# Kernel optimization log

Measured on AMD Instinct MI355X. Metric: run time of the kernel, lower is better.

The kernel has to match this reference:

```python
import jax, jax.numpy as jnp
import numpy as np

B, L, IN = 4, 2048, 64
D, N, K, NL, NC = 256, 16, 32, 2, 2


def _ln(x, g, b):
    m = x.mean(-1, keepdims=True)
    v = ((x - m) ** 2).mean(-1, keepdims=True)
    return (x - m) * jax.lax.rsqrt(v + 1e-5) * g + b


def _dwconv(x, w, b):
    # depthwise conv1d, kernel 3, padding 1; x: [B,L,D], w: [D,3]
    xp = jnp.pad(x, ((0, 0), (1, 1), (0, 0)))
    return xp[:, :-2] * w[:, 0] + xp[:, 1:-1] * w[:, 1] + xp[:, 2:] * w[:, 2] + b


def _ssm(x, loglam, wd, bd, wb, wc, wo, bo):
    # x: [B,L,D]
    lam = jax.nn.softplus(loglam)                      # [D,N]
    delta = jax.nn.softplus(x @ wd + bd)[..., None]    # [B,L,D,1]
    Bt = (x @ wb)[:, :, None, :]                       # [B,L,1,N]
    Ct = (x @ wc)[:, :, None, :]                       # [B,L,1,N]
    A_d = jnp.exp(-delta * lam)                        # [B,L,D,N]
    B_d = delta * Bt                                   # [B,L,D,N]
    A_l = jnp.moveaxis(A_d, 1, 0)                      # [L,B,D,N]
    B_l = jnp.moveaxis(B_d, 1, 0)

    def step(h, ab):
        a, b = ab
        h = a * h + b
        return h, h

    h0 = jnp.zeros((x.shape[0], D, N), x.dtype)
    _, hs = jax.lax.scan(step, h0, (A_l, B_l))         # [L,B,D,N]
    ys = hs * jnp.moveaxis(Ct, 1, 0)                   # [L,B,D,N]
    out = jnp.moveaxis(ys, 0, 1).reshape(x.shape[0], x.shape[1], D * N)
    return out @ wo + bo


def _temporal_block(x, lg, lb, cw, cb, loglam, wd, bd, wb, wc, wo, bo, gw, gb, pw, pb):
    res = x
    xn = _ln(x, lg, lb)
    xc = _dwconv(xn, cw, cb)
    xs = _ssm(xc, loglam, wd, bd, wb, wc, wo, bo)
    g = jax.nn.sigmoid(xn @ gw + gb)
    return (xs * g) @ pw + pb + res


def _spectral(x, fr, fi):
    X = jnp.fft.rfft(x, axis=1)                        # [B,F,D] complex64
    mag = jnp.abs(X).mean(axis=(0, 2))                 # [F]
    k = min(K, X.shape[1])
    _, idx = jax.lax.top_k(mag, k)
    filt = (fr[:, :k] + 1j * fi[:, :k]).T              # [k,D]
    Xk = X[:, idx, :] * filt[None]
    Xo = jnp.zeros(X.shape, X.dtype).at[:, idx, :].set(Xk)
    return jnp.fft.irfft(Xo, n=x.shape[1], axis=1)


def setup_inputs() -> dict:
    key = jax.random.key(0)
    ks = jax.random.split(key, 32)
    rn = lambda i, shape, s=0.02: jax.random.normal(ks[i], shape, jnp.float32) * s
    inp = {
        "x": jax.random.normal(ks[0], (B, L, IN), jnp.float32),
        "w_in": rn(1, (IN, D), 0.1), "b_in": jnp.zeros((D,), jnp.float32),
        "ln_g": jnp.ones((NL, D), jnp.float32), "ln_b": jnp.zeros((NL, D), jnp.float32),
        "conv_w": rn(2, (NL, D, 3), 0.3), "conv_b": jnp.zeros((NL, D), jnp.float32),
        "loglam": jax.random.uniform(ks[3], (NL, D, N), jnp.float32),
        "wd": rn(4, (NL, D, D), 0.05), "bd": jnp.zeros((NL, D), jnp.float32),
        "wb": rn(5, (NL, D, N), 0.05), "wc": rn(6, (NL, D, N), 0.05),
        "wo": rn(7, (NL, D * N, D), 0.01), "bo": jnp.zeros((NL, D), jnp.float32),
        "gate_w": rn(8, (NL, D, D), 0.05), "gate_b": jnp.zeros((NL, D), jnp.float32),
        "proj_w": rn(9, (NL, D, D), 0.05), "proj_b": jnp.zeros((NL, D), jnp.float32),
        "fr": rn(10, (D, K)), "fi": rn(11, (D, K)),
        "alpha": jnp.full((D,), 0.5, jnp.float32), "beta": jnp.full((D,), 0.5, jnp.float32),
        "g_out": jnp.ones((D,), jnp.float32), "b_out": jnp.zeros((D,), jnp.float32),
        "hw1": rn(12, (D, D // 2), 0.05), "hb1": jnp.zeros((D // 2,), jnp.float32),
        "hw2": rn(13, (D // 2, NC), 0.05), "hb2": jnp.zeros((NC,), jnp.float32),
    }
    return inp


def reference(x, w_in, b_in, ln_g, ln_b, conv_w, conv_b, loglam, wd, bd, wb, wc, wo, bo,
              gate_w, gate_b, proj_w, proj_b, fr, fi, alpha, beta, g_out, b_out,
              hw1, hb1, hw2, hb2):
    h = x @ w_in + b_in                                # [B,L,D]
    xt = h
    for i in range(NL):
        xt = _temporal_block(xt, ln_g[i], ln_b[i], conv_w[i], conv_b[i], loglam[i],
                             wd[i], bd[i], wb[i], wc[i], wo[i], bo[i],
                             gate_w[i], gate_b[i], proj_w[i], proj_b[i])
    xs = _spectral(h, fr, fi)
    z = alpha * xt + beta * xs
    z = _ln(z, g_out, b_out)
    zl = z[:, -1, :]                                   # [B,D]
    hid = jax.nn.silu(zl @ hw1 + hb1)                  # dropout is identity in eval
    return hid @ hw2 + hb2                             # [B,NC]
```

## Files before the change

### kernel.cpp

```cpp
#include <hip/hip_runtime.h>
#include <hip/hip_bf16.h>
#include <math.h>

#define BB   4
#define LL   2048
#define INF_ 64
#define DD   256
#define NN   16
#define KK   32
#define BLn  (BB*LL)
#define FCNT 1025
#define FSTR 1056
#define SKM  8192
#define SKN  256
#define PSZ  ((size_t)SKM * SKN)
#define IX(x) ((x) + ((x) >> 6))

typedef short short4v __attribute__((ext_vector_type(4)));
typedef short short8 __attribute__((ext_vector_type(8)));
typedef float f32x4  __attribute__((ext_vector_type(4)));

__device__ __forceinline__ float softplusf(float x) {
    return x > 20.f ? x : log1pf(__expf(x));
}
__device__ __forceinline__ float sigmoidf_(float x) {
    return 1.f / (1.f + __expf(-x));
}
__device__ __forceinline__ short bfs(float v) {
    __hip_bfloat16 h = __float2bfloat16(v);
    return *reinterpret_cast<short*>(&h);
}

__global__ void prep_kernel(const float* __restrict__ wd, const float* __restrict__ gw,
                            const float* __restrict__ pw, const float* __restrict__ wo,
                            const float* __restrict__ wb, const float* __restrict__ wc,
                            const float* __restrict__ w_in, float* __restrict__ tab,
                            __hip_bfloat16* __restrict__ cat0, __hip_bfloat16* __restrict__ cat1,
                            __hip_bfloat16* __restrict__ gwt, __hip_bfloat16* __restrict__ pwt,
                            __hip_bfloat16* __restrict__ wot, __hip_bfloat16* __restrict__ wint) {
    __shared__ float t[32][33];
    const int tid = threadIdx.x;
    int blk = blockIdx.x;
    if (blk < 8) {
        int i = blk * 256 + tid;
        if (i < 2048) {
            double ang = 2.0 * 3.14159265358979323846 * (double)i / 2048.0;
            tab[i]        = (float)cos(ang);
            tab[2048 + i] = (float)sin(ang);
        }
        return;
    }
    blk -= 8;
    const float* W; __hip_bfloat16* Wt; int K, N, bx, by;
    if (blk < 64)        { W = wd;                     Wt = cat0; K = 256;  N = 256; bx = blk & 7; by = blk >> 3; }
    else if (blk < 128)  { int q = blk - 64;  W = wd + 65536; Wt = cat1; K = 256; N = 256; bx = q & 7; by = q >> 3; }
    else if (blk < 192)  { int q = blk - 128; W = gw;  Wt = gwt;  K = 256;  N = 256; bx = q & 7; by = q >> 3; }
    else if (blk < 256)  { int q = blk - 192; W = pw;  Wt = pwt;  K = 256;  N = 256; bx = q & 7; by = q >> 3; }
    else if (blk < 1280) { int q = blk - 256; W = wo;  Wt = wot;  K = 4096; N = 256; bx = q & 7; by = q >> 3; }
    else if (blk < 1344) {
        int j = (blk - 1280) & 31;
        const float* src0 = (blk < 1312) ? wb : wb + DD * NN;
        const float* src1 = (blk < 1312) ? wc : wc + DD * NN;
        __hip_bfloat16* cat = (blk < 1312) ? cat0 : cat1;
        const float* src = (j < 16) ? src0 : src1;
        cat[(size_t)(256 + j) * 256 + tid] = __float2bfloat16(src[tid * 16 + (j & 15)]);
        return;
    } else { int q = blk - 1344; W = w_in; Wt = wint; K = 64; N = 256; bx = q & 7; by = q >> 3; }
    const int k0 = by * 32, n0 = bx * 32;
    if (k0 >= K) return;
    const int tx = tid & 31, ty = tid >> 5;
    for (int r = ty; r < 32; r += 8) t[r][tx] = W[(size_t)(k0 + r) * N + n0 + tx];
    __syncthreads();
    for (int r = ty; r < 32; r += 8)
        Wt[(size_t)(n0 + r) * K + k0 + tx] = __float2bfloat16(t[tx][r]);
}

__global__ __launch_bounds__(256)
void gemm_in_kernel(const float* __restrict__ x, const __hip_bfloat16* __restrict__ wint,
                    const float* __restrict__ b_in, float* __restrict__ h,
                    float* __restrict__ ht) {
    __shared__ alignas(16) short As[64][72];
    __shared__ alignas(16) short Bs[64][72];
    __shared__ float ts[64][68];
    const int tid = threadIdx.x;
    const int w = tid >> 6, lane = tid & 63;
    const int hi = lane >> 4, lo = lane & 15;
    const int row0 = blockIdx.y * 64, col0 = blockIdx.x * 64;
    const short* B = (const short*)wint;
#pragma unroll
    for (int e = 0; e < 4; ++e) {
        int q = e * 256 + tid;
        int r = q >> 4, c4 = (q & 15) * 4;
        float4 v = *(const float4*)&x[(size_t)(row0 + r) * 64 + c4];
        short4v s = {bfs(v.x), bfs(v.y), bfs(v.z), bfs(v.w)};
        *(short4v*)&As[r][c4] = s;
    }
#pragma unroll
    for (int e = 0; e < 2; ++e) {
        int q = e * 256 + tid;
        int r = q >> 3, c8 = (q & 7) * 8;
        *(short8*)&Bs[r][c8] = *(const short8*)&B[(size_t)(col0 + r) * 64 + c8];
    }
    __syncthreads();
    f32x4 acc[4];
    f32x4 zz = {0.f, 0.f, 0.f, 0.f};
#pragma unroll
    for (int n = 0; n < 4; ++n) acc[n] = zz;
#pragma unroll
    for (int s = 0; s < 2; ++s) {
        short8 af = *(const short8*)&As[w * 16 + lo][s * 32 + hi * 8];
#pragma unroll
        for (int n = 0; n < 4; ++n) {
            short8 bf = *(const short8*)&Bs[n * 16 + lo][s * 32 + hi * 8];
            acc[n] = __builtin_amdgcn_mfma_f32_16x16x32_bf16(af, bf, acc[n], 0, 0, 0);
        }
    }
#pragma unroll
    for (int n = 0; n < 4; ++n)
#pragma unroll
        for (int r = 0; r < 4; ++r) {
            const int row = row0 + w * 16 + hi * 4 + r;
            const int col = col0 + n * 16 + lo;
            float v = acc[n][r] + b_in[col];
            h[(size_t)row * 256 + col] = v;
            ts[n * 16 + lo][w * 16 + hi * 4 + r] = v;
        }
    __syncthreads();
    const int b = row0 >> 11, l0 = row0 & 2047, d0 = col0;
    const int dr = tid >> 2, seg = tid & 3;
    float* dst = ht + ((size_t)(b * 256 + d0 + dr)) * LL + l0 + seg * 16;
#pragma unroll
    for (int j = 0; j < 4; ++j)
        *(f32x4*)&dst[j * 4] = *(const f32x4*)&ts[dr][seg * 16 + j * 4];
}

__global__ __launch_bounds__(256)
void lnconv_kernel(const float* __restrict__ X, const float* __restrict__ g,
                   const float* __restrict__ bln, const float* __restrict__ cw,
                   const float* __restrict__ cb, __hip_bfloat16* __restrict__ xn_bf,
                   __hip_bfloat16* __restrict__ xc_bf) {
    __shared__ float xs[34][260];
    const int tid = threadIdx.x;
    const int w = tid >> 6, lane = tid & 63;
    const int blk = blockIdx.x;
    const int b = (blk * 32) >> 11, L0 = (blk * 32) & 2047;
    const float4 g4 = *(const float4*)&g[lane * 4];
    const float4 b4 = *(const float4*)&bln[lane * 4];
    for (int slot = w; slot < 34; slot += 4) {
        const int l = L0 - 1 + slot;
        if (l < 0 || l >= LL) {
            f32x4 z = {0.f, 0.f, 0.f, 0.f};
            *(f32x4*)&xs[slot][lane * 4] = z;
            continue;
        }
        float4 v = *(const float4*)&X[((size_t)b * LL + l) * DD + lane * 4];
        float s = v.x + v.y + v.z + v.w;
#pragma unroll
        for (int off = 1; off < 64; off <<= 1) s += __shfl_xor(s, off);
        float m = s * (1.f / DD);
        float cx = v.x - m, cy = v.y - m, cz = v.z - m, cw_ = v.w - m;
        float q = cx * cx + cy * cy + cz * cz + cw_ * cw_;
#pragma unroll
        for (int off = 1; off < 64; off <<= 1) q += __shfl_xor(q, off);
        float inv = rsqrtf(q * (1.f / DD) + 1e-5f);
        f32x4 y;
        y[0] = cx * inv * g4.x + b4.x;
        y[1] = cy * inv * g4.y + b4.y;
        y[2] = cz * inv * g4.z + b4.z;
        y[3] = cw_ * inv * g4.w + b4.w;
        *(f32x4*)&xs[slot][lane * 4] = y;
        if (slot >= 1 && slot <= 32) {
            short4v s4 = {bfs(y[0]), bfs(y[1]), bfs(y[2]), bfs(y[3])};
            *(short4v*)&xn_bf[((size_t)b * LL + l) * DD + lane * 4] = s4;
        }
    }
    __syncthreads();
    const int d = tid;
    const float w0 = cw[d * 3 + 0], w1 = cw[d * 3 + 1], w2 = cw[d * 3 + 2], cbd = cb[d];
    float xm = xs[0][d], x0 = xs[1][d];
    for (int rw = 0; rw < 32; ++rw) {
        float xp = xs[rw + 2][d];
        xc_bf[((size_t)b * LL + L0 + rw) * DD + d] =
            __float2bfloat16(fmaf(w0, xm, fmaf(w1, x0, fmaf(w2, xp, cbd))));
        xm = x0; x0 = xp;
    }
}

template<int MODE>
__global__ __launch_bounds__(256)
void gemm_core(const short* __restrict__ A, const short* __restrict__ Bw,
               const float* __restrict__ bias, const float* __restrict__ x1,
               const float* __restrict__ x2, float* __restrict__ o0,
               float* __restrict__ o1, float* __restrict__ o2,
               __hip_bfloat16* __restrict__ ob) {
    __shared__ alignas(16) short As[2][64][40];
    __shared__ alignas(16) short Bs[2][64][40];
    const int tid = threadIdx.x;
    const int w = tid >> 6, lane = tid & 63;
    const int hi = lane >> 4, lo = lane & 15;
    const int row0 = blockIdx.y * 64, col0 = blockIdx.x * 64;
    f32x4 acc[4];
    f32x4 zz = {0.f, 0.f, 0.f, 0.f};
#pragma unroll
    for (int n = 0; n < 4; ++n) acc[n] = zz;
    const int sr = tid >> 2, sc = (tid & 3) * 8;
    short8 pa = *(const short8*)&A[(size_t)(row0 + sr) * 256 + sc];
    short8 pb = *(const short8*)&Bw[(size_t)(col0 + sr) * 256 + sc];
    *(short8*)&As[0][sr][sc] = pa;
    *(short8*)&Bs[0][sr][sc] = pb;
    pa = *(const short8*)&A[(size_t)(row0 + sr) * 256 + 32 + sc];
    pb = *(const short8*)&Bw[(size_t)(col0 + sr) * 256 + 32 + sc];
    __syncthreads();
    int cur = 0;
    for (int it = 0; it < 8; ++it) {
        if (it + 1 < 8) {
            *(short8*)&As[cur ^ 1][sr][sc] = pa;
            *(short8*)&Bs[cur ^ 1][sr][sc] = pb;
        }
        if (it + 2 < 8) {
            const int k0 = (it + 2) << 5;
            pa = *(const short8*)&A[(size_t)(row0 + sr) * 256 + k0 + sc];
            pb = *(const short8*)&Bw[(size_t)(col0 + sr) * 256 + k0 + sc];
        }
        short8 af = *(const short8*)&As[cur][w * 16 + lo][hi * 8];
        short8 bfr[4];
#pragma unroll
        for (int n = 0; n < 4; ++n)
            bfr[n] = *(const short8*)&Bs[cur][n * 16 + lo][hi * 8];
#pragma unroll
        for (int n = 0; n < 4; ++n)
            acc[n] = __builtin_amdgcn_mfma_f32_16x16x32_bf16(af, bfr[n], acc[n], 0, 0, 0);
        __syncthreads();
        cur ^= 1;
    }
#pragma unroll
    for (int n = 0; n < 4; ++n) {
#pragma unroll
        for (int r = 0; r < 4; ++r) {
            const int row = row0 + w * 16 + hi * 4 + r;
            const int col = col0 + n * 16 + lo;
            float v = acc[n][r];
            if constexpr (MODE == 0) {
                if (col < 256)      o0[(size_t)row * 256 + col] = softplusf(v + bias[col]);
                else if (col < 272) o1[(size_t)row * 16 + col - 256] = v;
                else if (col < 288) o2[(size_t)row * 16 + col - 272] = v;
            } else if constexpr (MODE == 1) {
                float gv = sigmoidf_(v + bias[col]);
                float s = x1[(size_t)row * 256 + col] + x1[PSZ + (size_t)row * 256 + col] + x2[col];
                ob[(size_t)row * 256 + col] = __float2bfloat16(gv * s);
            } else {
                o0[(size_t)row * 256 + col] = v + bias[col] + x1[(size_t)row * 256 + col];
            }
        }
    }
}

__global__ __launch_bounds__(256)
void gemm_sk_kernel(const __hip_bfloat16* __restrict__ Abf, const __hip_bfloat16* __restrict__ Wt,
                    float* __restrict__ P) {
    __shared__ alignas(16) short As[2][128][72];
    __shared__ alignas(16) short Bs[2][64][72];
    const int tid = threadIdx.x;
    const int f = blockIdx.x;
    const int xcd = f & 7, slot = f >> 3;
    const int col = slot & 3;
    const int rk = xcd + (slot >> 2) * 8;
    const int row = rk & 63, kb = rk >> 6;
    const int row0 = row * 128, col0 = col * 64;
    const size_t kbase = (size_t)kb * 2048;
    const int w = tid >> 6, lane = tid & 63;
    const int hi = lane >> 4, lo = lane & 15;
    const short* A = (const short*)Abf;
    const short* B = (const short*)Wt;
    f32x4 acc[2][4];
    f32x4 zz = {0.f, 0.f, 0.f, 0.f};
#pragma unroll
    for (int m = 0; m < 2; ++m)
#pragma unroll
        for (int n = 0; n < 4; ++n) acc[m][n] = zz;
    const int sr = tid >> 3, sc = (tid & 7) * 8;
    const int sr1 = (256 + tid) >> 3, sc1 = ((256 + tid) & 7) * 8;
    const int sr2 = (512 + tid) >> 3, sc2 = ((512 + tid) & 7) * 8;
    const int sr3 = (768 + tid) >> 3, sc3 = ((768 + tid) & 7) * 8;
    short8 pa0 = *(const short8*)&A[(size_t)(row0 + sr ) * 4096 + kbase + sc ];
    short8 pa1 = *(const short8*)&A[(size_t)(row0 + sr1) * 4096 + kbase + sc1];
    short8 pa2 = *(const short8*)&A[(size_t)(row0 + sr2) * 4096 + kbase + sc2];
    short8 pa3 = *(const short8*)&A[(size_t)(row0 + sr3) * 4096 + kbase + sc3];
    short8 pb0 = *(const short8*)&B[(size_t)(col0 + sr ) * 4096 + kbase + sc ];
    short8 pb1 = *(const short8*)&B[(size_t)(col0 + sr1) * 4096 + kbase + sc1];
    *(short8*)&As[0][sr ][sc ] = pa0;
    *(short8*)&As[0][sr1][sc1] = pa1;
    *(short8*)&As[0][sr2][sc2] = pa2;
    *(short8*)&As[0][sr3][sc3] = pa3;
    *(short8*)&Bs[0][sr ][sc ] = pb0;
    *(short8*)&Bs[0][sr1][sc1] = pb1;
    {
        const size_t k0 = kbase + 64;
        pa0 = *(const short8*)&A[(size_t)(row0 + sr ) * 4096 + k0 + sc ];
        pa1 = *(const short8*)&A[(size_t)(row0 + sr1) * 4096 + k0 + sc1];
        pa2 = *(const short8*)&A[(size_t)(row0 + sr2) * 4096 + k0 + sc2];
        pa3 = *(const short8*)&A[(size_t)(row0 + sr3) * 4096 + k0 + sc3];
        pb0 = *(const short8*)&B[(size_t)(col0 + sr ) * 4096 + k0 + sc ];
        pb1 = *(const short8*)&B[(size_t)(col0 + sr1) * 4096 + k0 + sc1];
    }
    __syncthreads();
    int cur = 0;
    for (int it = 0; it < 32; ++it) {
        if (it + 1 < 32) {
            *(short8*)&As[cur ^ 1][sr ][sc ] = pa0;
            *(short8*)&As[cur ^ 1][sr1][sc1] = pa1;
            *(short8*)&As[cur ^ 1][sr2][sc2] = pa2;
            *(short8*)&As[cur ^ 1][sr3][sc3] = pa3;
            *(short8*)&Bs[cur ^ 1][sr ][sc ] = pb0;
            *(short8*)&Bs[cur ^ 1][sr1][sc1] = pb1;
        }
        if (it + 2 < 32) {
            const size_t k0 = kbase + (size_t)(it + 2) * 64;
            pa0 = *(const short8*)&A[(size_t)(row0 + sr ) * 4096 + k0 + sc ];
            pa1 = *(const short8*)&A[(size_t)(row0 + sr1) * 4096 + k0 + sc1];
            pa2 = *(const short8*)&A[(size_t)(row0 + sr2) * 4096 + k0 + sc2];
            pa3 = *(const short8*)&A[(size_t)(row0 + sr3) * 4096 + k0 + sc3];
            pb0 = *(const short8*)&B[(size_t)(col0 + sr ) * 4096 + k0 + sc ];
            pb1 = *(const short8*)&B[(size_t)(col0 + sr1) * 4096 + k0 + sc1];
        }
#pragma unroll
        for (int kk = 0; kk < 2; ++kk) {
            short8 af[2], bfr[4];
#pragma unroll
            for (int m = 0; m < 2; ++m)
                af[m] = *(const short8*)&As[cur][w * 32 + m * 16 + lo][kk * 32 + hi * 8];
#pragma unroll
            for (int n = 0; n < 4; ++n)
                bfr[n] = *(const short8*)&Bs[cur][n * 16 + lo][kk * 32 + hi * 8];
#pragma unroll
            for (int m = 0; m < 2; ++m)
#pragma unroll
                for (int n = 0; n < 4; ++n)
                    acc[m][n] = __builtin_amdgcn_mfma_f32_16x16x32_bf16(af[m], bfr[n], acc[m][n], 0, 0, 0);
        }
        __syncthreads();
        cur ^= 1;
    }
    float* Pk = P + (size_t)kb * PSZ;
#pragma unroll
    for (int m = 0; m < 2; ++m)
#pragma unroll
        for (int n = 0; n < 4; ++n)
#pragma unroll
            for (int r = 0; r < 4; ++r) {
                int rr = row0 + w * 32 + m * 16 + hi * 4 + r;
                int cc = col0 + n * 16 + lo;
                Pk[(size_t)rr * SKN + cc] = acc[m][n][r];
            }
}

template<int PHASE>
__global__ void ssm_chunk_kernel(const float* __restrict__ delta, const float* __restrict__ Bt,
                                 const float* __restrict__ Ct, const float* __restrict__ loglam,
                                 const float* __restrict__ hstart,
                                 float* __restrict__ sA, float* __restrict__ sB,
                                 __hip_bfloat16* __restrict__ ys) {
    __shared__ float dl[128][16];
    __shared__ float btl[128][16];
    __shared__ float ctl[128][16];
    const int dblk = blockIdx.x, c = blockIdx.y, b = blockIdx.z;
    const int tid = threadIdx.x;
    const size_t lbase = (size_t)b * LL + c * 128;
    for (int i = tid; i < 2048; i += 256) {
        int l = i >> 4, q = i & 15;
        dl[l][q]  = delta[(lbase + l) * DD + dblk * 16 + q];
        btl[l][q] = Bt[(lbase + l) * NN + q];
        if (PHASE == 1) ctl[l][q] = Ct[(lbase + l) * NN + q];
    }
    __syncthreads();
    const int dloc = tid >> 4, n = tid & 15;
    const float lam = softplusf(loglam[(dblk * 16 + dloc) * NN + n]);
    float hv = 0.f, ap = 1.f;
    if (PHASE == 1) hv = hstart[((size_t)(b * 16 + c)) * 4096 + dblk * 256 + tid];
    for (int l = 0; l < 128; ++l) {
        float dv = dl[l][dloc];
        float a = __expf(-dv * lam);
        hv = fmaf(a, hv, dv * btl[l][n]);
        if (PHASE == 0) ap *= a;
        else ys[(lbase + l) * (DD * NN) + dblk * 256 + tid] = __float2bfloat16(hv * ctl[l][n]);
    }
    if (PHASE == 0) {
        size_t oi = ((size_t)(b * 16 + c)) * 4096 + dblk * 256 + tid;
        sA[oi] = ap; sB[oi] = hv;
    }
}

__global__ void ssm_comb_kernel(const float* __restrict__ sA, const float* __restrict__ sB,
                                float* __restrict__ hstart, float* __restrict__ hfin) {
    const int id = blockIdx.x * 256 + threadIdx.x;
    const int b = id >> 12, col = id & 4095;
    float h = 0.f;
#pragma unroll
    for (int c = 0; c < 16; ++c) {
        size_t oi = ((size_t)(b * 16 + c)) * 4096 + col;
        hstart[oi] = h;
        h = fmaf(sA[oi], h, sB[oi]);
    }
    if (hfin) hfin[(size_t)b * 4096 + col] = h;
}

__global__ void last_ssm_part_kernel(const float* __restrict__ hfin, const float* __restrict__ Ct,
                                     const float* __restrict__ wo, float* __restrict__ part) {
    __shared__ float hC[4][128];
    const int c = blockIdx.x, tid = threadIdx.x;
    const int p0 = c * 128;
#pragma unroll
    for (int e = 0; e < 2; ++e) {
        int i = e * 256 + tid;
        int b = i >> 7, p = i & 127;
        hC[b][p] = hfin[b * 4096 + p0 + p] *
                   Ct[((size_t)b * LL + (LL - 1)) * NN + (p & 15)];
    }
    __syncthreads();
    float a0 = 0.f, a1 = 0.f, a2 = 0.f, a3 = 0.f;
    for (int p = 0; p < 128; ++p) {
        float wv = wo[(size_t)(p0 + p) * DD + tid];
        a0 = fmaf(hC[0][p], wv, a0);
        a1 = fmaf(hC[1][p], wv, a1);
        a2 = fmaf(hC[2][p], wv, a2);
        a3 = fmaf(hC[3][p], wv, a3);
    }
    part[(0 * 32 + c) * DD + tid] = a0;
    part[(1 * 32 + c) * DD + tid] = a1;
    part[(2 * 32 + c) * DD + tid] = a2;
    part[(3 * 32 + c) * DD + tid] = a3;
}

__global__ void last_redproj_kernel(const float* __restrict__ part, const float* __restrict__ bo,
                                    const __hip_bfloat16* __restrict__ xn, const float* __restrict__ gw,
                                    const float* __restrict__ gb, const float* __restrict__ pw,
                                    const float* __restrict__ pb, const float* __restrict__ resid,
                                    float* __restrict__ xtlast) {
    __shared__ float xrow[256];
    __shared__ float xsg[256];
    const int b = blockIdx.x, d = threadIdx.x;
    float ol = bo[d];
#pragma unroll
    for (int c = 0; c < 32; ++c) ol += part[(b * 32 + c) * DD + d];
    const size_t rbase = ((size_t)b * LL + (LL - 1)) * DD;
    xrow[d] = __bfloat162float(xn[rbase + d]);
    __syncthreads();
    float acc = gb[d];
    for (int k = 0; k < 256; ++k) acc = fmaf(xrow[k], gw[(size_t)k * DD + d], acc);
    xsg[d] = ol * sigmoidf_(acc);
    __syncthreads();
    float acc2 = pb[d];
    for (int k = 0; k < 256; ++k) acc2 = fmaf(xsg[k], pw[(size_t)k * DD + d], acc2);
    xtlast[b * DD + d] = acc2 + resid[rbase + d];
}

__global__ __launch_bounds__(256)
void fft2_kernel(const float* __restrict__ ht, const float* __restrict__ tab,
                 float* __restrict__ Xre, float* __restrict__ Xim) {
    __shared__ float re[2080];
    __shared__ float im[2080];
    __shared__ float c2[2048];
    __shared__ float s2[2048];
    const int tid = threadIdx.x;
    const int pair = blockIdx.x;
    const int b = pair >> 7, d0 = pair & 127;
    for (int p = tid; p < 2048; p += 256) {
        if (p >= 1) {
            int lh = 31 - __clz((unsigned)p);
            int j = p - (1 << lh);
            int t = j << (10 - lh);
            c2[p] = tab[t]; s2[p] = tab[2048 + t];
        }
    }
    const float* ha = ht + ((size_t)b * 256 + d0) * LL;
    const float* hb = ha + (size_t)128 * LL;
    for (int i = tid; i < 2048; i += 256) {
        int r = (int)(__brev((unsigned)i) >> 21);
        re[IX(r)] = ha[i];
        im[IX(r)] = hb[i];
    }
    __syncthreads();
#pragma unroll
    for (int s = 1; s <= 11; ++s) {
        const int half = 1 << (s - 1);
#pragma unroll
        for (int e = 0; e < 4; ++e) {
            int q = e * 256 + tid;
            int j = q & (half - 1);
            int i0 = ((q >> (s - 1)) << s) + j;
            int i1 = i0 + half;
            float wr = c2[half + j], wi = -s2[half + j];
            float xr = re[IX(i1)], xi = im[IX(i1)];
            float tr = xr * wr - xi * wi;
            float ti = xr * wi + xi * wr;
            float ur = re[IX(i0)], ui = im[IX(i0)];
            re[IX(i0)] = ur + tr; im[IX(i0)] = ui + ti;
            re[IX(i1)] = ur - tr; im[IX(i1)] = ui - ti;
        }
        __syncthreads();
    }
    const int seqa = b * 256 + d0;
    float* xra = Xre + (size_t)seqa * FSTR;
    float* xia = Xim + (size_t)seqa * FSTR;
    float* xrb = xra + (size_t)128 * FSTR;
    float* xib = xia + (size_t)128 * FSTR;
    for (int f = tid; f < FCNT; f += 256) {
        int nf = (2048 - f) & 2047;
        float zrf = re[IX(f)], zif = im[IX(f)];
        float zrn = re[IX(nf)], zin = im[IX(nf)];
        xra[f] = 0.5f * (zrf + zrn);
        xia[f] = 0.5f * (zif - zin);
        xrb[f] = 0.5f * (zif + zin);
        xib[f] = 0.5f * (zrn - zrf);
    }
}

__global__ void mag_part_kernel(const float* __restrict__ Xre, const float* __restrict__ Xim,
                                float* __restrict__ part) {
    const int fb = blockIdx.x, sb = blockIdx.y;
    const int tid = threadIdx.x;
    const int f = fb * 256 + tid;
    float s = 0.f;
    if (f < FCNT) {
        for (int q = 0; q < 64; ++q) {
            size_t base = (size_t)(sb * 64 + q) * FSTR + f;
            float re = Xre[base], im = Xim[base];
            s += sqrtf(re * re + im * im);
        }
    }
    part[sb * 1280 + fb * 256 + tid] = s;
}

__global__ void topk_kernel(const float* __restrict__ part, int* __restrict__ sel) {
    __shared__ float vals[1280];
    __shared__ float wv[4];
    __shared__ int wi[4];
    const int tid = threadIdx.x;
    const int lane = tid & 63, wid = tid >> 6;
    for (int i = tid; i < 1280; i += 256) {
        float v = -1e30f;
        if (i < FCNT) {
            v = 0.f;
#pragma unroll
            for (int sb = 0; sb < 16; ++sb) v += part[sb * 1280 + i];
        }
        vals[i] = v;
    }
    __syncthreads();
    for (int k = 0; k < 32; ++k) {
        float bv = -1e30f; int bi = 0x7fffffff;
        for (int i = tid; i < FCNT; i += 256) {
            float v = vals[i];
            if (v > bv) { bv = v; bi = i; }
        }
#pragma unroll
        for (int off = 32; off > 0; off >>= 1) {
            float ov = __shfl_down(bv, off);
            int   oi = __shfl_down(bi, off);
            if (ov > bv || (ov == bv && oi < bi)) { bv = ov; bi = oi; }
        }
        if (lane == 0) { wv[wid] = bv; wi[wid] = bi; }
        __syncthreads();
        if (tid == 0) {
            float fv = wv[0]; int fi = wi[0];
#pragma unroll
            for (int q = 1; q < 4; ++q)
                if (wv[q] > fv || (wv[q] == fv && wi[q] < fi)) { fv = wv[q]; fi = wi[q]; }
            sel[k] = fi;
            vals[fi] = -1e30f;
        }
        __syncthreads();
    }
}

__global__ void xslast_kernel(const float* __restrict__ Xre, const float* __restrict__ Xim,
                              const int* __restrict__ sel, const float* __restrict__ fr,
                              const float* __restrict__ fi, const float* __restrict__ tab,
                              float* __restrict__ xsl) {
    const int b = blockIdx.x, d = threadIdx.x;
    const size_t sbase = (size_t)(b * 256 + d) * FSTR;
    float acc = 0.f;
    for (int j = 0; j < 32; ++j) {
        int f = sel[j];
        float xr = Xre[sbase + f];
        float xi = Xim[sbase + f];
        float frv = fr[d * KK + j], fiv = fi[d * KK + j];
        float xor_ = xr * frv - xi * fiv;
        float xoi  = xr * fiv + xi * frv;
        int kk2 = (f * (LL - 1)) & (LL - 1);
        float c = tab[kk2], s = tab[2048 + kk2];
        float w = (f == 0 || f == 1024) ? 1.f : 2.f;
        acc = fmaf(w, xor_ * c - xoi * s, acc);
    }
    xsl[b * DD + d] = acc * (1.f / LL);
}

__global__ void head_kernel(const float* __restrict__ xtlast, const float* __restrict__ xslast,
                            const float* __restrict__ alpha, const float* __restrict__ beta,
                            const float* __restrict__ gout, const float* __restrict__ bout,
                            const float* __restrict__ hw1, const float* __restrict__ hb1,
                            const float* __restrict__ hw2, const float* __restrict__ hb2,
                            float* __restrict__ out) {
    __shared__ float red[256];
    __shared__ float z[256];
    __shared__ float hid[128];
    const int b = blockIdx.x, tid = threadIdx.x;
    float zv = alpha[tid] * xtlast[b * 256 + tid] + beta[tid] * xslast[b * 256 + tid];
    red[tid] = zv; __syncthreads();
    for (int s = 128; s > 0; s >>= 1) { if (tid < s) red[tid] += red[tid + s]; __syncthreads(); }
    float m = red[0] * (1.f / DD);
    __syncthreads();
    float c = zv - m;
    red[tid] = c * c; __syncthreads();
    for (int s = 128; s > 0; s >>= 1) { if (tid < s) red[tid] += red[tid + s]; __syncthreads(); }
    float var = red[0] * (1.f / DD);
    z[tid] = c * rsqrtf(var + 1e-5f) * gout[tid] + bout[tid];
    __syncthreads();
    if (tid < 128) {
        float a = hb1[tid];
        for (int k = 0; k < 256; ++k) a = fmaf(z[k], hw1[(size_t)k * 128 + tid], a);
        hid[tid] = a * sigmoidf_(a);
    }
    __syncthreads();
    if (tid < 2) {
        float a = hb2[tid];
        for (int k = 0; k < 128; ++k) a = fmaf(hid[k], hw2[(size_t)k * 2 + tid], a);
        out[b * 2 + tid] = a;
    }
}

extern "C" void kernel_launch(void* const* d_in, const int* in_sizes, int n_in,
                              void* d_out, int out_size, void* d_ws, size_t ws_size,
                              hipStream_t stream) {
    const float* x      = (const float*)d_in[0];
    const float* w_in   = (const float*)d_in[1];
    const float* b_in   = (const float*)d_in[2];
    const float* ln_g   = (const float*)d_in[3];
    const float* ln_b   = (const float*)d_in[4];
    const float* conv_w = (const float*)d_in[5];
    const float* conv_b = (const float*)d_in[6];
    const float* loglam = (const float*)d_in[7];
    const float* wd     = (const float*)d_in[8];
    const float* bd     = (const float*)d_in[9];
    const float* wb     = (const float*)d_in[10];
    const float* wc     = (const float*)d_in[11];
    const float* wo     = (const float*)d_in[12];
    const float* bo     = (const float*)d_in[13];
    const float* gw     = (const float*)d_in[14];
    const float* gb     = (const float*)d_in[15];
    const float* pw     = (const float*)d_in[16];
    const float* pb     = (const float*)d_in[17];
    const float* fr     = (const float*)d_in[18];
    const float* fi     = (const float*)d_in[19];
    const float* alpha  = (const float*)d_in[20];
    const float* beta   = (const float*)d_in[21];
    const float* gout   = (const float*)d_in[22];
    const float* bout   = (const float*)d_in[23];
    const float* hw1    = (const float*)d_in[24];
    const float* hb1    = (const float*)d_in[25];
    const float* hw2    = (const float*)d_in[26];
    const float* hb2    = (const float*)d_in[27];

    float* ws = (float*)d_ws;
    size_t o = 0;
    auto alloc = [&](size_t n) { float* p = ws + o; o += (n + 15) & ~(size_t)15; return p; };

    const size_t BLnDD = (size_t)BLn * DD;
    float* h      = alloc(BLnDD);
    float* xt1    = alloc(BLnDD);
    float* xpad   = alloc(BLnDD);
    float* ht     = alloc(BLnDD);
    float* delta  = alloc(BLnDD);
    float* Btm    = alloc((size_t)BLn * NN);
    float* Ctm    = alloc((size_t)BLn * NN);
    float* tab    = alloc(4096);
    float* ysf    = alloc(BLnDD * NN / 2);
    float* sA     = alloc((size_t)BB * 16 * 4096);
    float* sB     = alloc((size_t)BB * 16 * 4096);
    float* hst    = alloc((size_t)BB * 16 * 4096);
    float* xnbf_f = alloc(BLnDD / 2);
    float* xcbf_f = alloc(BLnDD / 2);
    float* xsgf   = alloc(BLnDD / 2);
    float* cat0_f = alloc((size_t)320 * 256 / 2);
    float* cat1_f = alloc((size_t)320 * 256 / 2);
    float* gwt_f  = alloc((size_t)DD * DD / 2);
    float* pwt_f  = alloc((size_t)DD * DD / 2);
    float* wot_f  = alloc((size_t)DD * NN * DD / 2);
    float* wint_f = alloc((size_t)DD * 64 / 2);
    float* magp   = alloc(16 * 1280);
    int*   sel    = (int*)alloc(32);
    float* hfin   = alloc((size_t)BB * DD * NN);
    float* lpart  = alloc((size_t)BB * 32 * DD);
    float* xtlast = alloc(BB * DD);
    float* xslast = alloc(BB * DD);

    __hip_bfloat16* ys    = (__hip_bfloat16*)ysf;
    float*          Xre   = ysf;
    float*          Xim   = ysf + (size_t)1024 * FSTR;
    __hip_bfloat16* xn_bf = (__hip_bfloat16*)xnbf_f;
    __hip_bfloat16* xc_bf = (__hip_bfloat16*)xcbf_f;
    __hip_bfloat16* xsg_bf= (__hip_bfloat16*)xsgf;
    __hip_bfloat16* cat0  = (__hip_bfloat16*)cat0_f;
    __hip_bfloat16* cat1  = (__hip_bfloat16*)cat1_f;
    __hip_bfloat16* gwt   = (__hip_bfloat16*)gwt_f;
    __hip_bfloat16* pwt   = (__hip_bfloat16*)pwt_f;
    __hip_bfloat16* wot   = (__hip_bfloat16*)wot_f;
    __hip_bfloat16* wint  = (__hip_bfloat16*)wint_f;
    float*          Pbuf  = xt1;

    const dim3 blk(256);

    prep_kernel<<<1368, blk, 0, stream>>>(wd, gw, pw, wo, wb, wc, w_in, tab,
                                          cat0, cat1, gwt, pwt, wot, wint);
    gemm_in_kernel<<<dim3(4, 128), blk, 0, stream>>>(x, wint, b_in, h, ht);

    const dim3 qgrid(5, BLn / 64);
    const dim3 ggrid(4, BLn / 64);
    const dim3 sgrid(16, 16, BB);

    lnconv_kernel<<<BLn / 32, blk, 0, stream>>>(h, ln_g, ln_b, conv_w, conv_b, xn_bf, xc_bf);
    gemm_core<0><<<qgrid, blk, 0, stream>>>((const short*)xc_bf, (const short*)cat0,
                                            bd, nullptr, nullptr, delta, Btm, Ctm, nullptr);
    ssm_chunk_kernel<0><<<sgrid, blk, 0, stream>>>(delta, Btm, nullptr, loglam,
                                                   nullptr, sA, sB, nullptr);
    ssm_comb_kernel<<<BB * 4096 / 256, blk, 0, stream>>>(sA, sB, hst, nullptr);
    ssm_chunk_kernel<1><<<sgrid, blk, 0, stream>>>(delta, Btm, Ctm, loglam,
                                                   hst, nullptr, nullptr, ys);
    gemm_sk_kernel<<<512, blk, 0, stream>>>(ys, wot, Pbuf);
    gemm_core<1><<<ggrid, blk, 0, stream>>>((const short*)xn_bf, (const short*)gwt,
                                            gb, Pbuf, bo, nullptr, nullptr, nullptr, xsg_bf);
    gemm_core<2><<<ggrid, blk, 0, stream>>>((const short*)xsg_bf, (const short*)pwt,
                                            pb, h, nullptr, xt1, nullptr, nullptr, nullptr);

    lnconv_kernel<<<BLn / 32, blk, 0, stream>>>(xt1, ln_g + DD, ln_b + DD,
                                                conv_w + DD * 3, conv_b + DD, xn_bf, xc_bf);
    gemm_core<0><<<qgrid, blk, 0, stream>>>((const short*)xc_bf, (const short*)cat1,
                                            bd + DD, nullptr, nullptr, delta, Btm, Ctm, nullptr);
    ssm_chunk_kernel<0><<<sgrid, blk, 0, stream>>>(delta, Btm, nullptr, loglam + DD * NN,
                                                   nullptr, sA, sB, nullptr);
    ssm_comb_kernel<<<BB * 4096 / 256, blk, 0, stream>>>(sA, sB, hst, hfin);
    last_ssm_part_kernel<<<32, blk, 0, stream>>>(hfin, Ctm, wo + (size_t)DD * NN * DD, lpart);
    last_redproj_kernel<<<BB, blk, 0, stream>>>(lpart, bo + DD, xn_bf,
                                                gw + (size_t)DD * DD, gb + DD,
                                                pw + (size_t)DD * DD, pb + DD, xt1, xtlast);

    fft2_kernel<<<512, blk, 0, stream>>>(ht, tab, Xre, Xim);
    mag_part_kernel<<<dim3(5, 16), blk, 0, stream>>>(Xre, Xim, magp);
    topk_kernel<<<1, blk, 0, stream>>>(magp, sel);
    xslast_kernel<<<BB, blk, 0, stream>>>(Xre, Xim, sel, fr, fi, tab, xslast);

    head_kernel<<<BB, blk, 0, stream>>>(xtlast, xslast, alpha, beta, gout, bout,
                                        hw1, hb1, hw2, hb2, (float*)d_out);
}
```

Before: 278.9 us.

## Widen split-K to four slices and fold chunk-combine and xslast kernels into consumers

The output-projection GEMM now splits K four ways with 32-wide k-tiles and 1024 blocks instead of two ways, and the gate epilogue sums four partial buffers held in a new dedicated buffer. The separate SSM chunk-combine kernel is removed: phase-1 chunk kernels and the last-step kernel each recompute the carried-in state serially from per-chunk sA/sB. The xslast kernel is merged into the head kernel. Together these aim to raise GEMM parallelism and cut launches, in exchange for redundant prefix recomputation and more partial-sum traffic.

New measurement: 282.1 us. About the same (+1.1%).

```diff
diff --git a/kernel.cpp b/kernel.cpp
--- a/kernel.cpp
+++ b/kernel.cpp
@@ -246,8 +246,9 @@
                 else if (col < 288) o2[(size_t)row * 16 + col - 272] = v;
             } else if constexpr (MODE == 1) {
                 float gv = sigmoidf_(v + bias[col]);
-                float s = x1[(size_t)row * 256 + col] + x1[PSZ + (size_t)row * 256 + col] + x2[col];
-                ob[(size_t)row * 256 + col] = __float2bfloat16(gv * s);
+                size_t idx = (size_t)row * 256 + col;
+                float s = x1[idx] + x1[PSZ + idx] + x1[2 * PSZ + idx] + x1[3 * PSZ + idx] + x2[col];
+                ob[idx] = __float2bfloat16(gv * s);
             } else {
                 o0[(size_t)row * 256 + col] = v + bias[col] + x1[(size_t)row * 256 + col];
             }
@@ -258,8 +259,8 @@
 __global__ __launch_bounds__(256)
 void gemm_sk_kernel(const __hip_bfloat16* __restrict__ Abf, const __hip_bfloat16* __restrict__ Wt,
                     float* __restrict__ P) {
-    __shared__ alignas(16) short As[2][128][72];
-    __shared__ alignas(16) short Bs[2][64][72];
+    __shared__ alignas(16) short As[2][128][40];
+    __shared__ alignas(16) short Bs[2][64][40];
     const int tid = threadIdx.x;
     const int f = blockIdx.x;
     const int xcd = f & 7, slot = f >> 3;
@@ -267,7 +268,7 @@
     const int rk = xcd + (slot >> 2) * 8;
     const int row = rk & 63, kb = rk >> 6;
     const int row0 = row * 128, col0 = col * 64;
-    const size_t kbase = (size_t)kb * 2048;
+    const size_t kbase = (size_t)kb * 1024;
     const int w = tid >> 6, lane = tid & 63;
     const int hi = lane >> 4, lo = lane & 15;
     const short* A = (const short*)Abf;
@@ -278,66 +279,43 @@
     for (int m = 0; m < 2; ++m)
 #pragma unroll
         for (int n = 0; n < 4; ++n) acc[m][n] = zz;
-    const int sr = tid >> 3, sc = (tid & 7) * 8;
-    const int sr1 = (256 + tid) >> 3, sc1 = ((256 + tid) & 7) * 8;
-    const int sr2 = (512 + tid) >> 3, sc2 = ((512 + tid) & 7) * 8;
-    const int sr3 = (768 + tid) >> 3, sc3 = ((768 + tid) & 7) * 8;
-    short8 pa0 = *(const short8*)&A[(size_t)(row0 + sr ) * 4096 + kbase + sc ];
-    short8 pa1 = *(const short8*)&A[(size_t)(row0 + sr1) * 4096 + kbase + sc1];
-    short8 pa2 = *(const short8*)&A[(size_t)(row0 + sr2) * 4096 + kbase + sc2];
-    short8 pa3 = *(const short8*)&A[(size_t)(row0 + sr3) * 4096 + kbase + sc3];
-    short8 pb0 = *(const short8*)&B[(size_t)(col0 + sr ) * 4096 + kbase + sc ];
-    short8 pb1 = *(const short8*)&B[(size_t)(col0 + sr1) * 4096 + kbase + sc1];
-    *(short8*)&As[0][sr ][sc ] = pa0;
-    *(short8*)&As[0][sr1][sc1] = pa1;
-    *(short8*)&As[0][sr2][sc2] = pa2;
-    *(short8*)&As[0][sr3][sc3] = pa3;
-    *(short8*)&Bs[0][sr ][sc ] = pb0;
-    *(short8*)&Bs[0][sr1][sc1] = pb1;
-    {
-        const size_t k0 = kbase + 64;
-        pa0 = *(const short8*)&A[(size_t)(row0 + sr ) * 4096 + k0 + sc ];
-        pa1 = *(const short8*)&A[(size_t)(row0 + sr1) * 4096 + k0 + sc1];
-        pa2 = *(const short8*)&A[(size_t)(row0 + sr2) * 4096 + k0 + sc2];
-        pa3 = *(const short8*)&A[(size_t)(row0 + sr3) * 4096 + k0 + sc3];
-        pb0 = *(const short8*)&B[(size_t)(col0 + sr ) * 4096 + k0 + sc ];
-        pb1 = *(const short8*)&B[(size_t)(col0 + sr1) * 4096 + k0 + sc1];
-    }
+    const int ra0 = tid >> 2,          ca0 = (tid & 3) * 8;
+    const int ra1 = (256 + tid) >> 2,  ca1 = ((256 + tid) & 3) * 8;
+    short8 pa0 = *(const short8*)&A[(size_t)(row0 + ra0) * 4096 + kbase + ca0];
+    short8 pa1 = *(const short8*)&A[(size_t)(row0 + ra1) * 4096 + kbase + ca1];
+    short8 pb  = *(const short8*)&B[(size_t)(col0 + ra0) * 4096 + kbase + ca0];
+    *(short8*)&As[0][ra0][ca0] = pa0;
+    *(short8*)&As[0][ra1][ca1] = pa1;
+    *(short8*)&Bs[0][ra0][ca0] = pb;
+    pa0 = *(const short8*)&A[(size_t)(row0 + ra0) * 4096 + kbase + 32 + ca0];
+    pa1 = *(const short8*)&A[(size_t)(row0 + ra1) * 4096 + kbase + 32 + ca1];
+    pb  = *(const short8*)&B[(size_t)(col0 + ra0) * 4096 + kbase + 32 + ca0];
     __syncthreads();
     int cur = 0;
     for (int it = 0; it < 32; ++it) {
         if (it + 1 < 32) {
-            *(short8*)&As[cur ^ 1][sr ][sc ] = pa0;
-            *(short8*)&As[cur ^ 1][sr1][sc1] = pa1;
-            *(short8*)&As[cur ^ 1][sr2][sc2] = pa2;
-            *(short8*)&As[cur ^ 1][sr3][sc3] = pa3;
-            *(short8*)&Bs[cur ^ 1][sr ][sc ] = pb0;
-            *(short8*)&Bs[cur ^ 1][sr1][sc1] = pb1;
+            *(short8*)&As[cur ^ 1][ra0][ca0] = pa0;
+            *(short8*)&As[cur ^ 1][ra1][ca1] = pa1;
+            *(short8*)&Bs[cur ^ 1][ra0][ca0] = pb;
         }
         if (it + 2 < 32) {
-            const size_t k0 = kbase + (size_t)(it + 2) * 64;
-            pa0 = *(const short8*)&A[(size_t)(row0 + sr ) * 4096 + k0 + sc ];
-            pa1 = *(const short8*)&A[(size_t)(row0 + sr1) * 4096 + k0 + sc1];
-            pa2 = *(const short8*)&A[(size_t)(row0 + sr2) * 4096 + k0 + sc2];
-            pa3 = *(const short8*)&A[(size_t)(row0 + sr3) * 4096 + k0 + sc3];
-            pb0 = *(const short8*)&B[(size_t)(col0 + sr ) * 4096 + k0 + sc ];
-            pb1 = *(const short8*)&B[(size_t)(col0 + sr1) * 4096 + k0 + sc1];
-        }
-#pragma unroll
-        for (int kk = 0; kk < 2; ++kk) {
-            short8 af[2], bfr[4];
-#pragma unroll
-            for (int m = 0; m < 2; ++m)
-                af[m] = *(const short8*)&As[cur][w * 32 + m * 16 + lo][kk * 32 + hi * 8];
+            const size_t k0 = kbase + ((it + 2) << 5);
+            pa0 = *(const short8*)&A[(size_t)(row0 + ra0) * 4096 + k0 + ca0];
+            pa1 = *(const short8*)&A[(size_t)(row0 + ra1) * 4096 + k0 + ca1];
+            pb  = *(const short8*)&B[(size_t)(col0 + ra0) * 4096 + k0 + ca0];
+        }
+        short8 af[2], bfr[4];
+#pragma unroll
+        for (int m = 0; m < 2; ++m)
+            af[m] = *(const short8*)&As[cur][w * 32 + m * 16 + lo][hi * 8];
+#pragma unroll
+        for (int n = 0; n < 4; ++n)
+            bfr[n] = *(const short8*)&Bs[cur][n * 16 + lo][hi * 8];
+#pragma unroll
+        for (int m = 0; m < 2; ++m)
 #pragma unroll
             for (int n = 0; n < 4; ++n)
-                bfr[n] = *(const short8*)&Bs[cur][n * 16 + lo][kk * 32 + hi * 8];
-#pragma unroll
-            for (int m = 0; m < 2; ++m)
-#pragma unroll
-                for (int n = 0; n < 4; ++n)
-                    acc[m][n] = __builtin_amdgcn_mfma_f32_16x16x32_bf16(af[m], bfr[n], acc[m][n], 0, 0, 0);
-        }
+                acc[m][n] = __builtin_amdgcn_mfma_f32_16x16x32_bf16(af[m], bfr[n], acc[m][n], 0, 0, 0);
         __syncthreads();
         cur ^= 1;
     }
@@ -357,7 +335,6 @@
 template<int PHASE>
 __global__ void ssm_chunk_kernel(const float* __restrict__ delta, const float* __restrict__ Bt,
                                  const float* __restrict__ Ct, const float* __restrict__ loglam,
-                                 const float* __restrict__ hstart,
                                  float* __restrict__ sA, float* __restrict__ sB,
                                  __hip_bfloat16* __restrict__ ys) {
     __shared__ float dl[128][16];
@@ -372,11 +349,16 @@
         btl[l][q] = Bt[(lbase + l) * NN + q];
         if (PHASE == 1) ctl[l][q] = Ct[(lbase + l) * NN + q];
     }
+    float hv = 0.f, ap = 1.f;
+    if (PHASE == 1) {
+        for (int cc = 0; cc < c; ++cc) {
+            size_t oi = ((size_t)(b * 16 + cc)) * 4096 + dblk * 256 + tid;
+            hv = fmaf(sA[oi], hv, sB[oi]);
+        }
+    }
     __syncthreads();
     const int dloc = tid >> 4, n = tid & 15;
     const float lam = softplusf(loglam[(dblk * 16 + dloc) * NN + n]);
-    float hv = 0.f, ap = 1.f;
-    if (PHASE == 1) hv = hstart[((size_t)(b * 16 + c)) * 4096 + dblk * 256 + tid];
     for (int l = 0; l < 128; ++l) {
         float dv = dl[l][dloc];
         float a = __expf(-dv * lam);
@@ -390,21 +372,8 @@
     }
 }
 
-__global__ void ssm_comb_kernel(const float* __restrict__ sA, const float* __restrict__ sB,
-                                float* __restrict__ hstart, float* __restrict__ hfin) {
-    const int id = blockIdx.x * 256 + threadIdx.x;
-    const int b = id >> 12, col = id & 4095;
-    float h = 0.f;
-#pragma unroll
-    for (int c = 0; c < 16; ++c) {
-        size_t oi = ((size_t)(b * 16 + c)) * 4096 + col;
-        hstart[oi] = h;
-        h = fmaf(sA[oi], h, sB[oi]);
-    }
-    if (hfin) hfin[(size_t)b * 4096 + col] = h;
-}
-
-__global__ void last_ssm_part_kernel(const float* __restrict__ hfin, const float* __restrict__ Ct,
+__global__ void last_ssm_part_kernel(const float* __restrict__ sA, const float* __restrict__ sB,
+                                     const float* __restrict__ Ct,
                                      const float* __restrict__ wo, float* __restrict__ part) {
     __shared__ float hC[4][128];
     const int c = blockIdx.x, tid = threadIdx.x;
@@ -413,8 +382,13 @@
     for (int e = 0; e < 2; ++e) {
         int i = e * 256 + tid;
         int b = i >> 7, p = i & 127;
-        hC[b][p] = hfin[b * 4096 + p0 + p] *
-                   Ct[((size_t)b * LL + (LL - 1)) * NN + (p & 15)];
+        float hh = 0.f;
+#pragma unroll
+        for (int cc = 0; cc < 16; ++cc) {
+            size_t oi = ((size_t)(b * 16 + cc)) * 4096 + p0 + p;
+            hh = fmaf(sA[oi], hh, sB[oi]);
+        }
+        hC[b][p] = hh * Ct[((size_t)b * LL + (LL - 1)) * NN + (p & 15)];
     }
     __syncthreads();
     float a0 = 0.f, a1 = 0.f, a2 = 0.f, a3 = 0.f;
@@ -573,29 +547,10 @@
     }
 }
 
-__global__ void xslast_kernel(const float* __restrict__ Xre, const float* __restrict__ Xim,
-                              const int* __restrict__ sel, const float* __restrict__ fr,
-                              const float* __restrict__ fi, const float* __restrict__ tab,
-                              float* __restrict__ xsl) {
-    const int b = blockIdx.x, d = threadIdx.x;
-    const size_t sbase = (size_t)(b * 256 + d) * FSTR;
-    float acc = 0.f;
-    for (int j = 0; j < 32; ++j) {
-        int f = sel[j];
-        float xr = Xre[sbase + f];
-        float xi = Xim[sbase + f];
-        float frv = fr[d * KK + j], fiv = fi[d * KK + j];
-        float xor_ = xr * frv - xi * fiv;
-        float xoi  = xr * fiv + xi * frv;
-        int kk2 = (f * (LL - 1)) & (LL - 1);
-        float c = tab[kk2], s = tab[2048 + kk2];
-        float w = (f == 0 || f == 1024) ? 1.f : 2.f;
-        acc = fmaf(w, xor_ * c - xoi * s, acc);
-    }
-    xsl[b * DD + d] = acc * (1.f / LL);
-}
-
-__global__ void head_kernel(const float* __restrict__ xtlast, const float* __restrict__ xslast,
+__global__ void head_kernel(const float* __restrict__ Xre, const float* __restrict__ Xim,
+                            const int* __restrict__ sel, const float* __restrict__ fr,
+                            const float* __restrict__ fi, const float* __restrict__ tab,
+                            const float* __restrict__ xtlast,
                             const float* __restrict__ alpha, const float* __restrict__ beta,
                             const float* __restrict__ gout, const float* __restrict__ bout,
                             const float* __restrict__ hw1, const float* __restrict__ hb1,
@@ -605,7 +560,22 @@
     __shared__ float z[256];
     __shared__ float hid[128];
     const int b = blockIdx.x, tid = threadIdx.x;
-    float zv = alpha[tid] * xtlast[b * 256 + tid] + beta[tid] * xslast[b * 256 + tid];
+    const size_t sbase = (size_t)(b * 256 + tid) * FSTR;
+    float xsl = 0.f;
+    for (int j = 0; j < 32; ++j) {
+        int f = sel[j];
+        float xr = Xre[sbase + f];
+        float xi = Xim[sbase + f];
+        float frv = fr[tid * KK + j], fiv = fi[tid * KK + j];
+        float xor_ = xr * frv - xi * fiv;
+        float xoi  = xr * fiv + xi * frv;
+        int kk2 = (f * (LL - 1)) & (LL - 1);
+        float c = tab[kk2], s = tab[2048 + kk2];
+        float w = (f == 0 || f == 1024) ? 1.f : 2.f;
+        xsl = fmaf(w, xor_ * c - xoi * s, xsl);
+    }
+    xsl *= (1.f / LL);
+    float zv = alpha[tid] * xtlast[b * 256 + tid] + beta[tid] * xsl;
     red[tid] = zv; __syncthreads();
     for (int s = 128; s > 0; s >>= 1) { if (tid < s) red[tid] += red[tid + s]; __syncthreads(); }
     float m = red[0] * (1.f / DD);
@@ -668,16 +638,15 @@
     const size_t BLnDD = (size_t)BLn * DD;
     float* h      = alloc(BLnDD);
     float* xt1    = alloc(BLnDD);
-    float* xpad   = alloc(BLnDD);
     float* ht     = alloc(BLnDD);
     float* delta  = alloc(BLnDD);
+    float* Pbuf   = alloc(4 * PSZ);
     float* Btm    = alloc((size_t)BLn * NN);
     float* Ctm    = alloc((size_t)BLn * NN);
     float* tab    = alloc(4096);
     float* ysf    = alloc(BLnDD * NN / 2);
     float* sA     = alloc((size_t)BB * 16 * 4096);
     float* sB     = alloc((size_t)BB * 16 * 4096);
-    float* hst    = alloc((size_t)BB * 16 * 4096);
     float* xnbf_f = alloc(BLnDD / 2);
     float* xcbf_f = alloc(BLnDD / 2);
     float* xsgf   = alloc(BLnDD / 2);
@@ -689,10 +658,8 @@
     float* wint_f = alloc((size_t)DD * 64 / 2);
     float* magp   = alloc(16 * 1280);
     int*   sel    = (int*)alloc(32);
-    float* hfin   = alloc((size_t)BB * DD * NN);
     float* lpart  = alloc((size_t)BB * 32 * DD);
     float* xtlast = alloc(BB * DD);
-    float* xslast = alloc(BB * DD);
 
     __hip_bfloat16* ys    = (__hip_bfloat16*)ysf;
     float*          Xre   = ysf;
@@ -706,7 +673,6 @@
     __hip_bfloat16* pwt   = (__hip_bfloat16*)pwt_f;
     __hip_bfloat16* wot   = (__hip_bfloat16*)wot_f;
     __hip_bfloat16* wint  = (__hip_bfloat16*)wint_f;
-    float*          Pbuf  = xt1;
 
     const dim3 blk(256);
 
@@ -722,11 +688,10 @@
     gemm_core<0><<<qgrid, blk, 0, stream>>>((const short*)xc_bf, (const short*)cat0,
                                             bd, nullptr, nullptr, delta, Btm, Ctm, nullptr);
     ssm_chunk_kernel<0><<<sgrid, blk, 0, stream>>>(delta, Btm, nullptr, loglam,
-                                                   nullptr, sA, sB, nullptr);
-    ssm_comb_kernel<<<BB * 4096 / 256, blk, 0, stream>>>(sA, sB, hst, nullptr);
+                                                   sA, sB, nullptr);
     ssm_chunk_kernel<1><<<sgrid, blk, 0, stream>>>(delta, Btm, Ctm, loglam,
-                                                   hst, nullptr, nullptr, ys);
-    gemm_sk_kernel<<<512, blk, 0, stream>>>(ys, wot, Pbuf);
+                                                   sA, sB, ys);
+    gemm_sk_kernel<<<1024, blk, 0, stream>>>(ys, wot, Pbuf);
     gemm_core<1><<<ggrid, blk, 0, stream>>>((const short*)xn_bf, (const short*)gwt,
                                             gb, Pbuf, bo, nullptr, nullptr, nullptr, xsg_bf);
     gemm_core<2><<<ggrid, blk, 0, stream>>>((const short*)xsg_bf, (const short*)pwt,
@@ -737,9 +702,8 @@
     gemm_core<0><<<qgrid, blk, 0, stream>>>((const short*)xc_bf, (const short*)cat1,
                                             bd + DD, nullptr, nullptr, delta, Btm, Ctm, nullptr);
     ssm_chunk_kernel<0><<<sgrid, blk, 0, stream>>>(delta, Btm, nullptr, loglam + DD * NN,
-                                                   nullptr, sA, sB, nullptr);
-    ssm_comb_kernel<<<BB * 4096 / 256, blk, 0, stream>>>(sA, sB, hst, hfin);
-    last_ssm_part_kernel<<<32, blk, 0, stream>>>(hfin, Ctm, wo + (size_t)DD * NN * DD, lpart);
+                                                   sA, sB, nullptr);
+    last_ssm_part_kernel<<<32, blk, 0, stream>>>(sA, sB, Ctm, wo + (size_t)DD * NN * DD, lpart);
     last_redproj_kernel<<<BB, blk, 0, stream>>>(lpart, bo + DD, xn_bf,
                                                 gw + (size_t)DD * DD, gb + DD,
                                                 pw + (size_t)DD * DD, pb + DD, xt1, xtlast);
@@ -747,8 +711,8 @@
     fft2_kernel<<<512, blk, 0, stream>>>(ht, tab, Xre, Xim);
     mag_part_kernel<<<dim3(5, 16), blk, 0, stream>>>(Xre, Xim, magp);
     topk_kernel<<<1, blk, 0, stream>>>(magp, sel);
-    xslast_kernel<<<BB, blk, 0, stream>>>(Xre, Xim, sel, fr, fi, tab, xslast);
-
-    head_kernel<<<BB, blk, 0, stream>>>(xtlast, xslast, alpha, beta, gout, bout,
+
+    head_kernel<<<BB, blk, 0, stream>>>(Xre, Xim, sel, fr, fi, tab, xtlast,
+                                        alpha, beta, gout, bout,
                                         hw1, hb1, hw2, hb2, (float*)d_out);
 }
```
